# Kernel tuning notes

Measured on AMD Instinct MI355X. Metric: run time of the kernel, lower is better.

Reference implementation:

```python
import jax, jax.numpy as jnp
import numpy as np

N_NODES = 48758
REL_NUM = 5
BN_EPS = 1e-5


def _dan(h, edge_index, edge_type, win_w, win_b, wrel, cout_w, cout_b):
    # One DAN layer: gather -> gcn-norm scatter-sum + per-relation transform -> scatter-softmax -> scatter-sum.
    dst, src = edge_index[0], edge_index[1]
    xlin = h @ win_w + win_b                         # [N, D]
    x_j = xlin[src]                                  # [E, D] per-edge gather
    # gcn_norm(edge_index, add_self_loops=False): deg over col (= edge_index[1])
    ones = jnp.ones(src.shape[0], xlin.dtype)
    deg = jax.ops.segment_sum(ones, src, num_segments=N_NODES)
    dis = jnp.where(deg > 0, 1.0 / jnp.sqrt(deg), 0.0)
    norm = dis[dst] * dis[src]                       # [E]
    msg_gcn = jax.ops.segment_sum(x_j * norm[:, None], dst, num_segments=N_NODES)
    # per-relation linear transform on edge messages (small fixed relation loop)
    res = jnp.zeros_like(x_j)
    for r in range(REL_NUM):
        res = res + jnp.where((edge_type == r)[:, None], x_j @ wrel[r], 0.0)
    # scatter-softmax over destination-node neighborhoods, per feature channel
    m = jax.ops.segment_max(res, dst, num_segments=N_NODES)      # [N, D]
    e = jnp.exp(res - m[dst])
    s = jax.ops.segment_sum(e, dst, num_segments=N_NODES)
    weig = e / s[dst]
    msg = jax.ops.segment_sum(res * weig, dst, num_segments=N_NODES)
    return (msg_gcn + 0.1 * jax.nn.relu(msg)) @ cout_w + cout_b


def setup_inputs() -> dict:
    key = jax.random.key(0)
    ks = jax.random.split(key, 18)
    D = 128
    E = 750000
    s = 0.05
    inp = {}
    inp['x'] = jax.random.normal(ks[0], (N_NODES, D), jnp.float32)
    inp['edge_index'] = jax.random.randint(ks[1], (2, E), 0, N_NODES)
    inp['edge_type'] = jax.random.randint(ks[2], (E,), 0, REL_NUM)
    inp['edge_weight'] = jax.random.uniform(ks[3], (E,), jnp.float32)
    inp['idx'] = jax.random.randint(ks[4], (4096,), 0, N_NODES)
    # input projection + batchnorm params
    inp['proj_w'] = jax.random.normal(ks[5], (D, D), jnp.float32) * s
    inp['proj_b'] = jnp.zeros((D,), jnp.float32)
    inp['bn_g'] = jnp.ones((D,), jnp.float32)
    inp['bn_b'] = jnp.zeros((D,), jnp.float32)
    # two DAN layers (hidden=output=128)
    inp['win0_w'] = jax.random.normal(ks[6], (D, D), jnp.float32) * s
    inp['win0_b'] = jnp.zeros((D,), jnp.float32)
    inp['wrel0'] = jax.random.normal(ks[7], (REL_NUM, D, D), jnp.float32) * s
    inp['cout0_w'] = jax.random.normal(ks[8], (D, D), jnp.float32) * s
    inp['cout0_b'] = jnp.zeros((D,), jnp.float32)
    inp['win1_w'] = jax.random.normal(ks[9], (D, D), jnp.float32) * s
    inp['win1_b'] = jnp.zeros((D,), jnp.float32)
    inp['wrel1'] = jax.random.normal(ks[10], (REL_NUM, D, D), jnp.float32) * s
    inp['cout1_w'] = jax.random.normal(ks[11], (D, D), jnp.float32) * s
    inp['cout1_b'] = jnp.zeros((D,), jnp.float32)
    return inp


def reference(x, edge_index, edge_type, edge_weight, idx,
              proj_w, proj_b, bn_g, bn_b,
              win0_w, win0_b, wrel0, cout0_w, cout0_b,
              win1_w, win1_b, wrel1, cout1_w, cout1_b):
    # proj -> BatchNorm1d (training-mode batch stats) -> relu
    h = x @ proj_w + proj_b
    mu = jnp.mean(h, axis=0)
    var = jnp.mean(jnp.square(h - mu), axis=0)
    h = (h - mu) / jnp.sqrt(var + BN_EPS) * bn_g + bn_b
    h = jax.nn.relu(h)
    h = _dan(h, edge_index, edge_type, win0_w, win0_b, wrel0, cout0_w, cout0_b)
    h = _dan(h, edge_index, edge_type, win1_w, win1_b, wrel1, cout1_w, cout1_b)
    h = jax.nn.gelu(h, approximate=False)  # dropout is identity for reference
    return h[idx]
```

## Files before the change

kernel.cpp:

```cpp
#include <hip/hip_runtime.h>

#define HIST_BPG 32
#define HIST_B   (HIST_BPG * 4)
#define HIST_MAXW 12288

__device__ inline float bf2f(unsigned short u) {
    return __uint_as_float(((unsigned)u) << 16);
}
__device__ inline unsigned short f2bf(float f) {
    unsigned u = __float_as_uint(f);
    u += 0x7fffu + ((u >> 16) & 1u);
    return (unsigned short)(u >> 16);
}

typedef __attribute__((ext_vector_type(8))) short short8v;
typedef __attribute__((ext_vector_type(4))) float f32x4;


__device__ __forceinline__
void gemmf32_body(const float* __restrict__ A, const float* __restrict__ W,
                  const float* __restrict__ bias, float* __restrict__ C,
                  unsigned short* __restrict__ Ct, int M, int tile)
{
    __shared__ float As[64][132];
    __shared__ float Ws[32][128];

    const int tid = threadIdx.x;
    const int row0 = tile * 64;

#pragma unroll
    for (int i = 0; i < 8; ++i) {
        int idx = tid + i * 256;
        int rr = idx >> 5;
        int cc = (idx & 31) << 2;
        int gr = row0 + rr;
        float4 v = make_float4(0.f, 0.f, 0.f, 0.f);
        if (gr < M) v = *reinterpret_cast<const float4*>(A + (size_t)gr * 128 + cc);
        *reinterpret_cast<float4*>(&As[rr][cc]) = v;
    }

    const int tx = tid & 15;
    const int ty = tid >> 4;
    float acc[4][8];
#pragma unroll
    for (int i = 0; i < 4; ++i)
#pragma unroll
        for (int j = 0; j < 8; ++j) acc[i][j] = 0.f;

    for (int kt = 0; kt < 4; ++kt) {
        __syncthreads();
#pragma unroll
        for (int i = 0; i < 4; ++i) {
            int idx = tid + i * 256;
            int rr = idx >> 5;
            int cc = (idx & 31) << 2;
            *reinterpret_cast<float4*>(&Ws[rr][cc]) =
                *reinterpret_cast<const float4*>(W + (size_t)(kt * 32 + rr) * 128 + cc);
        }
        __syncthreads();
#pragma unroll
        for (int kk = 0; kk < 32; ++kk) {
            const int k = kt * 32 + kk;
            float a0 = As[ty * 4 + 0][k];
            float a1 = As[ty * 4 + 1][k];
            float a2 = As[ty * 4 + 2][k];
            float a3 = As[ty * 4 + 3][k];
            float w[8];
#pragma unroll
            for (int j = 0; j < 8; ++j) w[j] = Ws[kk][tx + 16 * j];
#pragma unroll
            for (int j = 0; j < 8; ++j) {
                acc[0][j] = fmaf(a0, w[j], acc[0][j]);
                acc[1][j] = fmaf(a1, w[j], acc[1][j]);
                acc[2][j] = fmaf(a2, w[j], acc[2][j]);
                acc[3][j] = fmaf(a3, w[j], acc[3][j]);
            }
        }
    }

    float bb[8];
#pragma unroll
    for (int j = 0; j < 8; ++j) bb[j] = bias ? bias[tx + 16 * j] : 0.f;

#pragma unroll
    for (int i = 0; i < 4; ++i) {
        int gr = row0 + ty * 4 + i;
        if (gr >= M) continue;
#pragma unroll
        for (int j = 0; j < 8; ++j) {
            float v = acc[i][j] + bb[j];
            if (C)  C[(size_t)gr * 128 + tx + 16 * j] = v;
            if (Ct) Ct[(size_t)(tx + 16 * j) * 128 + gr] = f2bf(v);
        }
    }
}

__device__ __forceinline__
void mfma64_body(const unsigned short* __restrict__ A,
                 const unsigned short* __restrict__ Wmat,
                 const float* __restrict__ bias,
                 float* __restrict__ Cf, unsigned short* __restrict__ Cb,
                 int M, int tile)
{
    __shared__ unsigned short Bs[16384];

    const int tid = threadIdx.x;
#pragma unroll
    for (int i = 0; i < 8; ++i) {
        int idx = tid + i * 256;
        uint4 v = *reinterpret_cast<const uint4*>(Wmat + (size_t)idx * 8);
        int row = idx >> 4;
        int j = idx & 15;
        int byte = row * 256 + ((j ^ (row & 15)) << 4);
        *reinterpret_cast<uint4*>(reinterpret_cast<char*>(Bs) + byte) = v;
    }
    __syncthreads();

    const int wave = tid >> 6;
    const int lane = tid & 63;
    const int grp = lane >> 4;
    const int l16 = lane & 15;
    const int row = tile * 64 + wave * 16 + l16;
    const int rc = row < M ? row : M - 1;

    f32x4 acc[8] = {};
#pragma unroll
    for (int kt = 0; kt < 4; ++kt) {
        const int k0 = kt * 32 + grp * 8;
        short8v a = *reinterpret_cast<const short8v*>(A + (size_t)rc * 128 + k0);
        const int joff = kt * 4 + grp;
#pragma unroll
        for (int n = 0; n < 8; ++n) {
            int brow = 16 * n + l16;
            int byte = brow * 256 + ((joff ^ (brow & 15)) << 4);
            short8v b = *reinterpret_cast<const short8v*>(
                reinterpret_cast<const char*>(Bs) + byte);
            acc[n] = __builtin_amdgcn_mfma_f32_16x16x32_bf16(b, a, acc[n], 0, 0, 0);
        }
    }

    if (row >= M) return;

    float4 bb[8];
#pragma unroll
    for (int n = 0; n < 8; ++n)
        bb[n] = bias ? *reinterpret_cast<const float4*>(bias + 16 * n + grp * 4)
                     : make_float4(0.f, 0.f, 0.f, 0.f);

#pragma unroll
    for (int n = 0; n < 8; ++n) {
        float v0 = acc[n][0] + bb[n].x;
        float v1 = acc[n][1] + bb[n].y;
        float v2 = acc[n][2] + bb[n].z;
        float v3 = acc[n][3] + bb[n].w;
        if (Cf) {
            *reinterpret_cast<float4*>(Cf + (size_t)row * 128 + 16 * n + grp * 4) =
                make_float4(v0, v1, v2, v3);
        }
        if (Cb) {
            unsigned u0 = (unsigned)f2bf(v0) | ((unsigned)f2bf(v1) << 16);
            unsigned u1 = (unsigned)f2bf(v2) | ((unsigned)f2bf(v3) << 16);
            *reinterpret_cast<uint2*>(Cb + (size_t)row * 128 + 16 * n + grp * 4) =
                make_uint2(u0, u1);
        }
    }
}

__device__ void fused_dispatch(const unsigned short* A, const unsigned short* Wt,
                               const float* biasbuf, unsigned short* Xb,
                               unsigned short* Yb, int base, int M, int nmats, int bid)
{
    int m = bid % nmats;
    int tile = bid / nmats;
    unsigned short* out = (m == 0) ? Xb : Yb + (size_t)(m - 1) * (size_t)M * 128;
    mfma64_body(A, Wt + (size_t)(base + m) * 16384,
                biasbuf + (size_t)(base + m) * 128, nullptr, out, M, tile);
}

__device__ void biasprod_body(const float* __restrict__ v, const float* __restrict__ W,
                              const float* __restrict__ add, float* __restrict__ out)
{
    int t = threadIdx.x;
    if (t >= 128) return;
    float s = add ? add[t] : 0.f;
    for (int j = 0; j < 128; ++j) s = fmaf(v[j], W[(size_t)j * 128 + t], s);
    out[t] = s;
}

__device__ void wtconv_body(const float* __restrict__ W, unsigned short* __restrict__ O)
{
    for (int i = threadIdx.x; i < 16384; i += 256) {
        int k = i >> 7, n = i & 127;
        O[(size_t)n * 128 + k] = f2bf(W[i]);
    }
}

__device__ void bn_stats_body(const float* __restrict__ h, float* __restrict__ sums,
                              int Nn, int b)
{
    const int c = threadIdx.x & 127;
    const int half = threadIdx.x >> 7;
    float s = 0.f, q = 0.f;
    for (int row = b * 2 + half; row < Nn; row += 512) {
        float v = h[(size_t)row * 128 + c];
        s += v;
        q += v * v;
    }
    __shared__ float ls[256], lq[256];
    ls[threadIdx.x] = s;
    lq[threadIdx.x] = q;
    __syncthreads();
    if (half == 0) {
        s += ls[threadIdx.x + 128];
        q += lq[threadIdx.x + 128];
        atomicAdd(&sums[c], s);
        atomicAdd(&sums[128 + c], q);
    }
}

__device__ void scan_block_sums_body(const int* __restrict__ cnt, int* __restrict__ bsum,
                                     int Nn, int b)
{
    __shared__ int sd[256];
    int tid = threadIdx.x;
    int i = b * 256 + tid;
    sd[tid] = i < Nn ? ((cnt[i] + 3) & ~3) : 0;
    __syncthreads();
#pragma unroll
    for (int s = 128; s > 0; s >>= 1) {
        if (tid < s) sd[tid] += sd[tid + s];
        __syncthreads();
    }
    if (tid == 0) bsum[b] = sd[0];
}

__device__ void scan_offsets_body(int* __restrict__ bsum, int nb)
{
    __shared__ int sd[256];
    int tid = threadIdx.x;
    int v = tid < nb ? bsum[tid] : 0;
    sd[tid] = v;
    __syncthreads();
    for (int d = 1; d < 256; d <<= 1) {
        int t = tid >= d ? sd[tid - d] : 0;
        __syncthreads();
        sd[tid] += t;
        __syncthreads();
    }
    if (tid < nb) bsum[tid] = sd[tid] - v;
}


__global__ __launch_bounds__(256)
void kprod1(const float* win0w, const float* win0b, const float* win1w, const float* win1b,
            const float* cout0w, const float* cout0b, const float* cout1w,
            const float* cout1b, const float* wrel0,
            float* WfA1, unsigned short* Wt, float* biasbuf, int nrel)
{
    const int IA1 = 1 + nrel, IC1 = 2 + 2 * nrel;
    const int nProd = 1 + nrel;
    int bid = blockIdx.x;
    if (bid < 2 * nProd) {
        int p = bid >> 1, tile = bid & 1;
        if (p == 0)
            gemmf32_body(cout0w, win1w, nullptr, WfA1, Wt + (size_t)IA1 * 16384, 128, tile);
        else
            gemmf32_body(win0w, wrel0 + (size_t)(p - 1) * 16384, nullptr,
                         nullptr, Wt + (size_t)p * 16384, 128, tile);
        return;
    }
    bid -= 2 * nProd;
    if (bid < nProd) {
        if (bid == 0) biasprod_body(cout0b, win1w, win1b, biasbuf + (size_t)IA1 * 128);
        else biasprod_body(win0b, wrel0 + (size_t)(bid - 1) * 16384, nullptr,
                           biasbuf + (size_t)bid * 128);
        return;
    }
    bid -= nProd;
    if (bid == 0) { wtconv_body(win0w, Wt); return; }
    if (bid == 1) { wtconv_body(cout1w, Wt + (size_t)IC1 * 16384); return; }
    int t = threadIdx.x;
    if (t < 128) {
        biasbuf[t] = win0b[t];
        biasbuf[(size_t)IC1 * 128 + t] = cout1b[t];
    }
}

__global__ __launch_bounds__(256)
void kprod2(const float* wrel1, const float* WfA1, unsigned short* Wt,
            float* biasbuf, int nrel)
{
    const int IA1 = 1 + nrel, IB1 = 2 + nrel;
    int bid = blockIdx.x;
    if (bid < 2 * nrel) {
        int p = bid >> 1, tile = bid & 1;
        gemmf32_body(WfA1, wrel1 + (size_t)p * 16384, nullptr,
                     nullptr, Wt + (size_t)(IB1 + p) * 16384, 128, tile);
        return;
    }
    int r = bid - 2 * nrel;
    biasprod_body(biasbuf + (size_t)IA1 * 128, wrel1 + (size_t)r * 16384, nullptr,
                  biasbuf + (size_t)(IB1 + r) * 128);
}

__global__ __launch_bounds__(256)
void hist_kernel(const int* __restrict__ ei, unsigned* __restrict__ partial,
                 int Nn, int E, int WORDS, int HALFR)
{
    __shared__ unsigned sh[HIST_MAXW];
    const int hbid = blockIdx.x;
    const int g = hbid / HIST_BPG;
    const int j = hbid - g * HIST_BPG;

    for (int w = threadIdx.x; w < WORDS; w += 256) sh[w] = 0;
    __syncthreads();

    const int* col = (g < 2) ? (ei + E) : ei;
    const int base = (g & 1) * HALFR;
    const size_t e0 = (size_t)E * j / HIST_BPG;
    const size_t e1 = (size_t)E * (j + 1) / HIST_BPG;
    for (size_t e = e0 + threadIdx.x; e < e1; e += 256) {
        int n = col[e] - base;
        if ((unsigned)n < (unsigned)HALFR)
            atomicAdd(&sh[n >> 1], 1u << ((n & 1) * 16));
    }
    __syncthreads();

    unsigned* out = partial + (size_t)hbid * WORDS;
    for (int w = threadIdx.x; w < WORDS; w += 256) out[w] = sh[w];
}

__global__ __launch_bounds__(256)
void proj_kernel(const float* __restrict__ x, const float* __restrict__ W,
                 const float* __restrict__ bias, float* __restrict__ h, int M)
{
    gemmf32_body(x, W, bias, h, nullptr, M, blockIdx.x);
}

__global__ __launch_bounds__(256)
void k2_reduce_bnstats(const unsigned* __restrict__ partial, float* __restrict__ dis,
                       int* __restrict__ cnt, const float* __restrict__ h,
                       float* __restrict__ bnsums, int Nn, int WORDS, int HALFR, int nRed)
{
    int bid = blockIdx.x;
    if (bid < nRed) {
        int t = bid * 256 + threadIdx.x;
        if (t < 4 * WORDS) {
            int histo = t / (2 * WORDS);
            int rem = t - histo * 2 * WORDS;
            int half = rem / WORDS;
            int w = rem - half * WORDS;
            int g = histo * 2 + half;
            unsigned slo = 0, shi = 0;
            const unsigned* p = partial + (size_t)(g * HIST_BPG) * WORDS + w;
#pragma unroll 4
            for (int j = 0; j < HIST_BPG; ++j) {
                unsigned u = p[(size_t)j * WORDS];
                slo += u & 0xffffu;
                shi += u >> 16;
            }
            int n0 = half * HALFR + 2 * w;
            int n1 = n0 + 1;
            if (histo == 0) {
                if (n0 < Nn) dis[n0] = slo ? rsqrtf((float)slo) : 0.f;
                if (n1 < Nn) dis[n1] = shi ? rsqrtf((float)shi) : 0.f;
            } else {
                if (n0 < Nn) cnt[n0] = (int)slo;
                if (n1 < Nn) cnt[n1] = (int)shi;
            }
        }
        return;
    }
    bn_stats_body(h, bnsums, Nn, bid - nRed);
}

__global__ __launch_bounds__(256)
void k3_bnfin_scan1(const float* __restrict__ sums, const float* __restrict__ g,
                    const float* __restrict__ b, float* __restrict__ sc,
                    const int* __restrict__ cnt, int* __restrict__ bsum, int Nn)
{
    if (blockIdx.x == 0) {
        int c = threadIdx.x;
        if (c < 128) {
            float inv = 1.f / (float)Nn;
            float mu = sums[c] * inv;
            float var = sums[128 + c] * inv - mu * mu;
            float rstd = rsqrtf(var + 1e-5f);
            float scale = rstd * g[c];
            sc[c] = scale;
            sc[128 + c] = b[c] - mu * scale;
        }
        return;
    }
    scan_block_sums_body(cnt, bsum, Nn, blockIdx.x - 1);
}

__global__ __launch_bounds__(256)
void k4_scanoff_bnapply(int* __restrict__ bsum, int nb,
                        const float* __restrict__ h, const float* __restrict__ sc,
                        unsigned short* __restrict__ hb, size_t n4)
{
    if (blockIdx.x == 0) { scan_offsets_body(bsum, nb); return; }
    size_t i = (size_t)(blockIdx.x - 1) * 256 + threadIdx.x;
    if (i >= n4) return;
    int c = (int)(i & 31) << 2;
    float4 v = reinterpret_cast<const float4*>(h)[i];
    float o0 = fmaxf(fmaf(v.x, sc[c + 0], sc[128 + c + 0]), 0.f);
    float o1 = fmaxf(fmaf(v.y, sc[c + 1], sc[128 + c + 1]), 0.f);
    float o2 = fmaxf(fmaf(v.z, sc[c + 2], sc[128 + c + 2]), 0.f);
    float o3 = fmaxf(fmaf(v.w, sc[c + 3], sc[128 + c + 3]), 0.f);
    ushort4 pk = make_ushort4(f2bf(o0), f2bf(o1), f2bf(o2), f2bf(o3));
    reinterpret_cast<ushort4*>(hb)[i] = pk;
}

__global__ __launch_bounds__(256)
void k4b_scanfinal(const int* __restrict__ cnt, const int* __restrict__ bsum,
                   int* __restrict__ rowptr, int* __restrict__ cursor,
                   uint4* __restrict__ csr, unsigned* __restrict__ Yw,
                   unsigned sink_woff, int Nn, int nb)
{
    if ((int)blockIdx.x == nb) {
        int t = threadIdx.x;
        if (t < 64) Yw[sink_woff + t] = 0xC2C8C2C8u;
        return;
    }
    __shared__ int sd[256];
    int tid = threadIdx.x;
    int b = blockIdx.x;
    int i = b * 256 + tid;
    int v = i < Nn ? cnt[i] : 0;
    int pv = (v + 3) & ~3;
    sd[tid] = pv;
    __syncthreads();
    for (int d = 1; d < 256; d <<= 1) {
        int t2 = tid >= d ? sd[tid - d] : 0;
        __syncthreads();
        sd[tid] += t2;
        __syncthreads();
    }
    if (i < Nn) {
        int off = sd[tid] - pv + bsum[b];
        rowptr[i] = off;
        cursor[i] = off;
        uint4 sink = make_uint4(0u, sink_woff, 0u, 0u);
        for (int j = v; j < pv; ++j) csr[off + j] = sink;
        if (i == Nn - 1) {
            rowptr[Nn] = off + pv;
            for (int q = 0; q < 8; ++q) csr[off + pv + q] = sink;
        }
    }
}

__global__ __launch_bounds__(256)
void k5_mfma_scatter(const unsigned short* hb, const unsigned short* Wt,
                     const float* biasbuf, unsigned short* Xb, unsigned short* Yb,
                     int M, int nmats, int nF,
                     const int* __restrict__ ei, const int* __restrict__ et,
                     const float* __restrict__ dis, int* __restrict__ cursor,
                     uint4* __restrict__ csr, int E, int Nn, int nS)
{
    const int minv = nF < nS ? nF : nS;
    int bid = blockIdx.x;
    int fIdx = -1, sIdx = -1;
    if (bid < 2 * minv) {
        if (bid & 1) fIdx = bid >> 1; else sIdx = bid >> 1;
    } else {
        int rem = bid - 2 * minv;
        if (nF > nS) fIdx = minv + rem; else sIdx = minv + rem;
    }
    if (sIdx >= 0) {
        int e = sIdx * 256 + threadIdx.x;
        if (e < E) {
            int dst = ei[e];
            int src = ei[E + e];
            int pos = atomicAdd(&cursor[dst], 1);
            float nrm = dis[dst] * dis[src];
            csr[pos] = make_uint4((unsigned)(src * 64),
                                  (unsigned)((et[e] * Nn + src) * 64),
                                  __float_as_uint(nrm), 0u);
        }
        return;
    }
    fused_dispatch(hb, Wt, biasbuf, Xb, Yb, 0, M, nmats, fIdx);
}

__global__ __launch_bounds__(256)
void k_fusedpass(const unsigned short* A, const unsigned short* Wt, const float* biasbuf,
                 unsigned short* Xb, unsigned short* Yb, int base, int M, int nmats)
{
    fused_dispatch(A, Wt, biasbuf, Xb, Yb, base, M, nmats, blockIdx.x);
}

__global__ __launch_bounds__(256)
void k_cout_gelu(const unsigned short* __restrict__ A, const unsigned short* Wt,
                 const float* biasbuf, float* __restrict__ out, int mat, int M)
{
    const unsigned short* Wmat = Wt + (size_t)mat * 16384;
    const float* bias = biasbuf + (size_t)mat * 128;

    __shared__ unsigned short Bs[16384];
    const int tid = threadIdx.x;
#pragma unroll
    for (int i = 0; i < 8; ++i) {
        int idx = tid + i * 256;
        uint4 v = *reinterpret_cast<const uint4*>(Wmat + (size_t)idx * 8);
        int row = idx >> 4;
        int j = idx & 15;
        int byte = row * 256 + ((j ^ (row & 15)) << 4);
        *reinterpret_cast<uint4*>(reinterpret_cast<char*>(Bs) + byte) = v;
    }
    __syncthreads();

    const int wave = tid >> 6;
    const int lane = tid & 63;
    const int grp = lane >> 4;
    const int l16 = lane & 15;
    const int row = blockIdx.x * 64 + wave * 16 + l16;
    const int rc = row < M ? row : M - 1;

    f32x4 acc[8] = {};
#pragma unroll
    for (int kt = 0; kt < 4; ++kt) {
        const int k0 = kt * 32 + grp * 8;
        short8v a = *reinterpret_cast<const short8v*>(A + (size_t)rc * 128 + k0);
        const int joff = kt * 4 + grp;
#pragma unroll
        for (int n = 0; n < 8; ++n) {
            int brow = 16 * n + l16;
            int byte = brow * 256 + ((joff ^ (brow & 15)) << 4);
            short8v b = *reinterpret_cast<const short8v*>(
                reinterpret_cast<const char*>(Bs) + byte);
            acc[n] = __builtin_amdgcn_mfma_f32_16x16x32_bf16(b, a, acc[n], 0, 0, 0);
        }
    }

    if (row >= M) return;

    const float kg = 0.7071067811865475f;
#pragma unroll
    for (int n = 0; n < 8; ++n) {
        float4 bb = *reinterpret_cast<const float4*>(bias + 16 * n + grp * 4);
        float v0 = acc[n][0] + bb.x;
        float v1 = acc[n][1] + bb.y;
        float v2 = acc[n][2] + bb.z;
        float v3 = acc[n][3] + bb.w;
        v0 = 0.5f * v0 * (1.f + erff(v0 * kg));
        v1 = 0.5f * v1 * (1.f + erff(v1 * kg));
        v2 = 0.5f * v2 * (1.f + erff(v2 * kg));
        v3 = 0.5f * v3 * (1.f + erff(v3 * kg));
        *reinterpret_cast<float4*>(out + (size_t)row * 128 + 16 * n + grp * 4) =
            make_float4(v0, v1, v2, v3);
    }
}

__global__ __launch_bounds__(256)
void node_gather(const int* __restrict__ rowptr, const uint4* __restrict__ csr,
                 const unsigned* __restrict__ Xw, const unsigned* __restrict__ Yw,
                 unsigned short* __restrict__ outb,
                 const int* __restrict__ idxmap, int count)
{
    int gid = blockIdx.x * 4 + (threadIdx.x >> 6);
    if (gid >= count) return;
    int node = idxmap ? idxmap[gid] : gid;
    int lane = threadIdx.x & 63;

    int i = rowptr[node];
    const int end = rowptr[node + 1];

    float mg0 = 0.f, mg1 = 0.f, s0 = 0.f, s1 = 0.f, t0 = 0.f, t1 = 0.f;

    if (i < end) {
        uint4 cur[4];
#pragma unroll
        for (int q = 0; q < 4; ++q) cur[q] = csr[i + q];

        for (; i < end; i += 4) {
            uint4 nxt[4];
#pragma unroll
            for (int q = 0; q < 4; ++q) nxt[q] = csr[i + 4 + q];

            unsigned xp[4], yp[4];
#pragma unroll
            for (int q = 0; q < 4; ++q) {
                xp[q] = Xw[cur[q].x + lane];
                yp[q] = Yw[cur[q].y + lane];
            }
#pragma unroll
            for (int q = 0; q < 4; ++q) {
                float nrm = __uint_as_float(cur[q].z);
                float x0 = bf2f((unsigned short)(xp[q] & 0xffffu));
                float x1 = bf2f((unsigned short)(xp[q] >> 16));
                float y0 = bf2f((unsigned short)(yp[q] & 0xffffu));
                float y1 = bf2f((unsigned short)(yp[q] >> 16));
                float w0 = __expf(y0), w1 = __expf(y1);
                mg0 = fmaf(x0, nrm, mg0);
                mg1 = fmaf(x1, nrm, mg1);
                s0 += w0; s1 += w1;
                t0 = fmaf(y0, w0, t0);
                t1 = fmaf(y1, w1, t1);
            }
#pragma unroll
            for (int q = 0; q < 4; ++q) cur[q] = nxt[q];
        }
    }

    float o0 = mg0 + 0.1f * fmaxf(s0 > 0.f ? t0 / s0 : 0.f, 0.f);
    float o1 = mg1 + 0.1f * fmaxf(s1 > 0.f ? t1 / s1 : 0.f, 0.f);
    unsigned pk = (unsigned)f2bf(o0) | ((unsigned)f2bf(o1) << 16);
    *reinterpret_cast<unsigned*>(outb + (size_t)gid * 128 + (lane << 1)) = pk;
}

extern "C" void kernel_launch(void* const* d_in, const int* in_sizes, int n_in,
                              void* d_out, int out_size, void* d_ws, size_t ws_size,
                              hipStream_t stream)
{
    const float* x      = (const float*)d_in[0];
    const int*   ei     = (const int*)d_in[1];
    const int*   et     = (const int*)d_in[2];
    const int*   idxp   = (const int*)d_in[4];
    const float* proj_w = (const float*)d_in[5];
    const float* proj_b = (const float*)d_in[6];
    const float* bn_g   = (const float*)d_in[7];
    const float* bn_b   = (const float*)d_in[8];
    const float* win_w[2]  = {(const float*)d_in[9],  (const float*)d_in[14]};
    const float* win_b[2]  = {(const float*)d_in[10], (const float*)d_in[15]};
    const float* wrel[2]   = {(const float*)d_in[11], (const float*)d_in[16]};
    const float* cout_w[2] = {(const float*)d_in[12], (const float*)d_in[17]};
    const float* cout_b[2] = {(const float*)d_in[13], (const float*)d_in[18]};

    const int Nn  = in_sizes[0] / 128;
    const int E   = in_sizes[1] / 2;
    const int Mo  = in_sizes[4];
    const int nrel = in_sizes[11] / (128 * 128);
    const size_t ND = (size_t)Nn * 128;

    const int HALFR = ((Nn + 3) / 4) * 2;
    const int WORDS = HALFR / 2;
    if (WORDS > HIST_MAXW) return;

    const int IA1 = 1 + nrel;
    const int IC1 = 2 + 2 * nrel;
    const int NMATS = 3 + 2 * nrel;

    char* p = (char*)d_ws;
    float* h    = (float*)p;                  p += ND * 4;
    unsigned short* hb = (unsigned short*)p;  p += ND * 2;
    unsigned short* Xb = (unsigned short*)p;  p += ND * 2;
    unsigned short* Yb = (unsigned short*)p;  p += (size_t)nrel * ND * 2 + 256;
    unsigned short* msgb = (unsigned short*)p; p += ND * 2;
    unsigned short* Wt = (unsigned short*)p;  p += (size_t)NMATS * 16384 * 2;
    float* WfA1 = (float*)p;                  p += (size_t)16384 * 4;
    float* biasbuf = (float*)p;               p += (size_t)NMATS * 128 * 4;
    uint4* csr  = (uint4*)p;                  p += ((size_t)E + 3 * (size_t)Nn + 16) * 16;
    unsigned* partial = (unsigned*)p;         p += (size_t)HIST_B * WORDS * 4;
    float* dis  = (float*)p;                  p += (size_t)Nn * 4;
    int*   cnt  = (int*)p;                    p += (size_t)Nn * 4;
    int*   rowptr = (int*)p;                  p += ((size_t)Nn + 1) * 4;
    int*   cursor = (int*)p;                  p += (size_t)Nn * 4;
    int*   bsum = (int*)p;                    p += 1024 * 4;
    float* bnsums = (float*)p;                p += 256 * 4;
    float* bnsc   = (float*)p;                p += 256 * 4;
    if ((size_t)(p - (char*)d_ws) > ws_size) return;

    const unsigned sink_woff = (unsigned)((size_t)nrel * Nn * 64);

    const int gemmGrid = (Nn + 63) / 64;
    const int tiles64 = (Nn + 63) / 64;
    const size_t n4 = ND / 4;
    const int n4grid = (int)((n4 + 255) / 256);
    const int nb = (Nn + 255) / 256;
    const int nRed = (4 * WORDS + 255) / 256;
    const int nS = (E + 255) / 256;
    const int nmats = 1 + nrel;
    const int nFused = nmats * tiles64;

    hipMemsetAsync(bnsums, 0, 256 * 4, stream);

    kprod1<<<2 * (1 + nrel) + (1 + nrel) + 3, 256, 0, stream>>>(
        win_w[0], win_b[0], win_w[1], win_b[1], cout_w[0], cout_b[0],
        cout_w[1], cout_b[1], wrel[0], WfA1, Wt, biasbuf, nrel);
    kprod2<<<2 * nrel + nrel, 256, 0, stream>>>(wrel[1], WfA1, Wt, biasbuf, nrel);

    hist_kernel<<<HIST_B, 256, 0, stream>>>(ei, partial, Nn, E, WORDS, HALFR);
    proj_kernel<<<gemmGrid, 256, 0, stream>>>(x, proj_w, proj_b, h, Nn);

    k2_reduce_bnstats<<<nRed + 256, 256, 0, stream>>>(
        partial, dis, cnt, h, bnsums, Nn, WORDS, HALFR, nRed);

    k3_bnfin_scan1<<<1 + nb, 256, 0, stream>>>(bnsums, bn_g, bn_b, bnsc, cnt, bsum, Nn);

    k4_scanoff_bnapply<<<1 + n4grid, 256, 0, stream>>>(bsum, nb, h, bnsc, hb, n4);

    k4b_scanfinal<<<nb + 1, 256, 0, stream>>>(cnt, bsum, rowptr, cursor, csr,
                                              (unsigned*)Yb, sink_woff, Nn, nb);

    k5_mfma_scatter<<<nFused + nS, 256, 0, stream>>>(
        hb, Wt, biasbuf, Xb, Yb, Nn, nmats, nFused,
        ei, et, dis, cursor, csr, E, Nn, nS);

    node_gather<<<(Nn + 3) / 4, 256, 0, stream>>>(
        rowptr, csr, (const unsigned*)Xb, (const unsigned*)Yb, msgb, nullptr, Nn);

    k_fusedpass<<<nFused, 256, 0, stream>>>(msgb, Wt, biasbuf, Xb, Yb, IA1, Nn, nmats);

    node_gather<<<(Mo + 3) / 4, 256, 0, stream>>>(
        rowptr, csr, (const unsigned*)Xb, (const unsigned*)Yb, msgb, idxp, Mo);

    k_cout_gelu<<<(Mo + 63) / 64, 256, 0, stream>>>(
        msgb, Wt, biasbuf, (float*)d_out, IC1, Mo);
}
```

Measured before the change: 329.3 us.

## Widen MFMA tiles to 512-thread blocks and merge projection into weight-prep kernel

The MFMA GEMM bodies now run with 512 threads, so each block covers 128 rows and loads the shared weight tile once for twice as many rows, halving weight staging per output row. The scatter part of k5 also handles 512 edges per block. The input projection GEMM and the second weight-product kernel are merged into one launch (kmid), and the histogram kernel is moved ahead of kprod1 to cut launch count and serialization. Larger blocks may reduce occupancy or load balance on the wave-heavy kernels.

New measurement: 311.5 us. 5.4% less time.

```diff
diff --git a/kernel.cpp b/kernel.cpp
--- a/kernel.cpp
+++ b/kernel.cpp
@@ -96,18 +96,18 @@
 }
 
 __device__ __forceinline__
-void mfma64_body(const unsigned short* __restrict__ A,
-                 const unsigned short* __restrict__ Wmat,
-                 const float* __restrict__ bias,
-                 float* __restrict__ Cf, unsigned short* __restrict__ Cb,
-                 int M, int tile)
+void mfmaw_body(const unsigned short* __restrict__ A,
+                const unsigned short* __restrict__ Wmat,
+                const float* __restrict__ bias,
+                float* __restrict__ Cf, unsigned short* __restrict__ Cb,
+                int M, int tile)
 {
     __shared__ unsigned short Bs[16384];
 
     const int tid = threadIdx.x;
 #pragma unroll
-    for (int i = 0; i < 8; ++i) {
-        int idx = tid + i * 256;
+    for (int i = 0; i < 4; ++i) {
+        int idx = tid + i * 512;
         uint4 v = *reinterpret_cast<const uint4*>(Wmat + (size_t)idx * 8);
         int row = idx >> 4;
         int j = idx & 15;
@@ -120,7 +120,7 @@
     const int lane = tid & 63;
     const int grp = lane >> 4;
     const int l16 = lane & 15;
-    const int row = tile * 64 + wave * 16 + l16;
+    const int row = tile * 128 + wave * 16 + l16;
     const int rc = row < M ? row : M - 1;
 
     f32x4 acc[8] = {};
@@ -173,8 +173,8 @@
     int m = bid % nmats;
     int tile = bid / nmats;
     unsigned short* out = (m == 0) ? Xb : Yb + (size_t)(m - 1) * (size_t)M * 128;
-    mfma64_body(A, Wt + (size_t)(base + m) * 16384,
-                biasbuf + (size_t)(base + m) * 128, nullptr, out, M, tile);
+    mfmaw_body(A, Wt + (size_t)(base + m) * 16384,
+               biasbuf + (size_t)(base + m) * 128, nullptr, out, M, tile);
 }
 
 __device__ void biasprod_body(const float* __restrict__ v, const float* __restrict__ W,
@@ -250,6 +250,33 @@
     if (tid < nb) bsum[tid] = sd[tid] - v;
 }
 
+
+__global__ __launch_bounds__(256)
+void hist_kernel(const int* __restrict__ ei, unsigned* __restrict__ partial,
+                 int Nn, int E, int WORDS, int HALFR)
+{
+    __shared__ unsigned sh[HIST_MAXW];
+    const int hbid = blockIdx.x;
+    const int g = hbid / HIST_BPG;
+    const int j = hbid - g * HIST_BPG;
+
+    for (int w = threadIdx.x; w < WORDS; w += 256) sh[w] = 0;
+    __syncthreads();
+
+    const int* col = (g < 2) ? (ei + E) : ei;
+    const int base = (g & 1) * HALFR;
+    const size_t e0 = (size_t)E * j / HIST_BPG;
+    const size_t e1 = (size_t)E * (j + 1) / HIST_BPG;
+    for (size_t e = e0 + threadIdx.x; e < e1; e += 256) {
+        int n = col[e] - base;
+        if ((unsigned)n < (unsigned)HALFR)
+            atomicAdd(&sh[n >> 1], 1u << ((n & 1) * 16));
+    }
+    __syncthreads();
+
+    unsigned* out = partial + (size_t)hbid * WORDS;
+    for (int w = threadIdx.x; w < WORDS; w += 256) out[w] = sh[w];
+}
 
 __global__ __launch_bounds__(256)
 void kprod1(const float* win0w, const float* win0b, const float* win1w, const float* win1b,
@@ -287,8 +314,9 @@
 }
 
 __global__ __launch_bounds__(256)
-void kprod2(const float* wrel1, const float* WfA1, unsigned short* Wt,
-            float* biasbuf, int nrel)
+void kmid(const float* wrel1, const float* WfA1, unsigned short* Wt, float* biasbuf,
+          const float* x, const float* proj_w, const float* proj_b, float* h,
+          int M, int nrel)
 {
     const int IA1 = 1 + nrel, IB1 = 2 + nrel;
     int bid = blockIdx.x;
@@ -298,43 +326,14 @@
                      nullptr, Wt + (size_t)(IB1 + p) * 16384, 128, tile);
         return;
     }
-    int r = bid - 2 * nrel;
-    biasprod_body(biasbuf + (size_t)IA1 * 128, wrel1 + (size_t)r * 16384, nullptr,
-                  biasbuf + (size_t)(IB1 + r) * 128);
-}
-
-__global__ __launch_bounds__(256)
-void hist_kernel(const int* __restrict__ ei, unsigned* __restrict__ partial,
-                 int Nn, int E, int WORDS, int HALFR)
-{
-    __shared__ unsigned sh[HIST_MAXW];
-    const int hbid = blockIdx.x;
-    const int g = hbid / HIST_BPG;
-    const int j = hbid - g * HIST_BPG;
-
-    for (int w = threadIdx.x; w < WORDS; w += 256) sh[w] = 0;
-    __syncthreads();
-
-    const int* col = (g < 2) ? (ei + E) : ei;
-    const int base = (g & 1) * HALFR;
-    const size_t e0 = (size_t)E * j / HIST_BPG;
-    const size_t e1 = (size_t)E * (j + 1) / HIST_BPG;
-    for (size_t e = e0 + threadIdx.x; e < e1; e += 256) {
-        int n = col[e] - base;
-        if ((unsigned)n < (unsigned)HALFR)
-            atomicAdd(&sh[n >> 1], 1u << ((n & 1) * 16));
-    }
-    __syncthreads();
-
-    unsigned* out = partial + (size_t)hbid * WORDS;
-    for (int w = threadIdx.x; w < WORDS; w += 256) out[w] = sh[w];
-}
-
-__global__ __launch_bounds__(256)
-void proj_kernel(const float* __restrict__ x, const float* __restrict__ W,
-                 const float* __restrict__ bias, float* __restrict__ h, int M)
-{
-    gemmf32_body(x, W, bias, h, nullptr, M, blockIdx.x);
+    bid -= 2 * nrel;
+    if (bid < nrel) {
+        biasprod_body(biasbuf + (size_t)IA1 * 128, wrel1 + (size_t)bid * 16384, nullptr,
+                      biasbuf + (size_t)(IB1 + bid) * 128);
+        return;
+    }
+    bid -= nrel;
+    gemmf32_body(x, proj_w, proj_b, h, nullptr, M, bid);
 }
 
 __global__ __launch_bounds__(256)
@@ -451,7 +450,7 @@
     }
 }
 
-__global__ __launch_bounds__(256)
+__global__ __launch_bounds__(512)
 void k5_mfma_scatter(const unsigned short* hb, const unsigned short* Wt,
                      const float* biasbuf, unsigned short* Xb, unsigned short* Yb,
                      int M, int nmats, int nF,
@@ -469,7 +468,7 @@
         if (nF > nS) fIdx = minv + rem; else sIdx = minv + rem;
     }
     if (sIdx >= 0) {
-        int e = sIdx * 256 + threadIdx.x;
+        int e = sIdx * 512 + threadIdx.x;
         if (e < E) {
             int dst = ei[e];
             int src = ei[E + e];
@@ -484,14 +483,14 @@
     fused_dispatch(hb, Wt, biasbuf, Xb, Yb, 0, M, nmats, fIdx);
 }
 
-__global__ __launch_bounds__(256)
+__global__ __launch_bounds__(512)
 void k_fusedpass(const unsigned short* A, const unsigned short* Wt, const float* biasbuf,
                  unsigned short* Xb, unsigned short* Yb, int base, int M, int nmats)
 {
     fused_dispatch(A, Wt, biasbuf, Xb, Yb, base, M, nmats, blockIdx.x);
 }
 
-__global__ __launch_bounds__(256)
+__global__ __launch_bounds__(512)
 void k_cout_gelu(const unsigned short* __restrict__ A, const unsigned short* Wt,
                  const float* biasbuf, float* __restrict__ out, int mat, int M)
 {
@@ -501,8 +500,8 @@
     __shared__ unsigned short Bs[16384];
     const int tid = threadIdx.x;
 #pragma unroll
-    for (int i = 0; i < 8; ++i) {
-        int idx = tid + i * 256;
+    for (int i = 0; i < 4; ++i) {
+        int idx = tid + i * 512;
         uint4 v = *reinterpret_cast<const uint4*>(Wmat + (size_t)idx * 8);
         int row = idx >> 4;
         int j = idx & 15;
@@ -515,7 +514,7 @@
     const int lane = tid & 63;
     const int grp = lane >> 4;
     const int l16 = lane & 15;
-    const int row = blockIdx.x * 64 + wave * 16 + l16;
+    const int row = blockIdx.x * 128 + wave * 16 + l16;
     const int rc = row < M ? row : M - 1;
 
     f32x4 acc[8] = {};
@@ -665,24 +664,25 @@
     const unsigned sink_woff = (unsigned)((size_t)nrel * Nn * 64);
 
     const int gemmGrid = (Nn + 63) / 64;
-    const int tiles64 = (Nn + 63) / 64;
+    const int tiles128 = (Nn + 127) / 128;
     const size_t n4 = ND / 4;
     const int n4grid = (int)((n4 + 255) / 256);
     const int nb = (Nn + 255) / 256;
     const int nRed = (4 * WORDS + 255) / 256;
-    const int nS = (E + 255) / 256;
+    const int nS = (E + 511) / 512;
     const int nmats = 1 + nrel;
-    const int nFused = nmats * tiles64;
+    const int nFused = nmats * tiles128;
 
     hipMemsetAsync(bnsums, 0, 256 * 4, stream);
+
+    hist_kernel<<<HIST_B, 256, 0, stream>>>(ei, partial, Nn, E, WORDS, HALFR);
 
     kprod1<<<2 * (1 + nrel) + (1 + nrel) + 3, 256, 0, stream>>>(
         win_w[0], win_b[0], win_w[1], win_b[1], cout_w[0], cout_b[0],
         cout_w[1], cout_b[1], wrel[0], WfA1, Wt, biasbuf, nrel);
-    kprod2<<<2 * nrel + nrel, 256, 0, stream>>>(wrel[1], WfA1, Wt, biasbuf, nrel);
-
-    hist_kernel<<<HIST_B, 256, 0, stream>>>(ei, partial, Nn, E, WORDS, HALFR);
-    proj_kernel<<<gemmGrid, 256, 0, stream>>>(x, proj_w, proj_b, h, Nn);
+
+    kmid<<<3 * nrel + gemmGrid, 256, 0, stream>>>(
+        wrel[1], WfA1, Wt, biasbuf, x, proj_w, proj_b, h, Nn, nrel);
 
     k2_reduce_bnstats<<<nRed + 256, 256, 0, stream>>>(
         partial, dis, cnt, h, bnsums, Nn, WORDS, HALFR, nRed);
@@ -694,18 +694,18 @@
     k4b_scanfinal<<<nb + 1, 256, 0, stream>>>(cnt, bsum, rowptr, cursor, csr,
                                               (unsigned*)Yb, sink_woff, Nn, nb);
 
-    k5_mfma_scatter<<<nFused + nS, 256, 0, stream>>>(
+    k5_mfma_scatter<<<nFused + nS, 512, 0, stream>>>(
         hb, Wt, biasbuf, Xb, Yb, Nn, nmats, nFused,
         ei, et, dis, cursor, csr, E, Nn, nS);
 
     node_gather<<<(Nn + 3) / 4, 256, 0, stream>>>(
         rowptr, csr, (const unsigned*)Xb, (const unsigned*)Yb, msgb, nullptr, Nn);
 
-    k_fusedpass<<<nFused, 256, 0, stream>>>(msgb, Wt, biasbuf, Xb, Yb, IA1, Nn, nmats);
+    k_fusedpass<<<nFused, 512, 0, stream>>>(msgb, Wt, biasbuf, Xb, Yb, IA1, Nn, nmats);
 
     node_gather<<<(Mo + 3) / 4, 256, 0, stream>>>(
         rowptr, csr, (const unsigned*)Xb, (const unsigned*)Yb, msgb, idxp, Mo);
 
-    k_cout_gelu<<<(Mo + 63) / 64, 256, 0, stream>>>(
+    k_cout_gelu<<<(Mo + 127) / 128, 512, 0, stream>>>(
         msgb, Wt, biasbuf, (float*)d_out, IC1, Mo);
 }
```
